# Kernel optimization log

Measured on AMD Instinct MI355X. Metric: run time of the kernel, lower is better.

## Reference

```python
import jax, jax.numpy as jnp
from jax import lax
import numpy as np

KSIZE = 3      # match-patch size
STRIDE = 1
RATE = 2       # down/up-sampling rate
FUSE_K = 3
SCALE = 10.0   # softmax scale
DN = ('NHWC', 'HWIO', 'NHWC')


def extract_patches(x, k, s):
    """tf.image.extract_patches(..., padding='SAME'); returns [B, L, k, k, C]."""
    B, H, W, C = x.shape
    oh, ow = -(-H // s), -(-W // s)
    ph = max((oh - 1) * s + k - H, 0)
    pw = max((ow - 1) * s + k - W, 0)
    xp = jnp.pad(x, ((0, 0), (ph // 2, ph - ph // 2), (pw // 2, pw - pw // 2), (0, 0)))
    cols = [xp[:, i:i + oh * s:s, j:j + ow * s:s, :] for i in range(k) for j in range(k)]
    p = jnp.stack(cols, axis=3)                 # [B, oh, ow, k*k, C]
    return p.reshape(B, oh * ow, k, k, C)


def setup_inputs() -> dict:
    key = jax.random.key(0)
    k1, k2, k3 = jax.random.split(key, 3)
    B, H, W, C = 4, 96, 96, 64
    f = jax.random.normal(k1, (B, H, W, C), jnp.float32)
    b = jax.random.normal(k2, (B, H, W, C), jnp.float32)
    mask = jnp.zeros((B, H, W, 1), jnp.float32)          # 0 = no hole -> all patches valid
    fuse_weight = jax.random.normal(k3, (FUSE_K, FUSE_K, 1, 1), jnp.float32) * 0.3
    return {"f": f, "b": b, "mask": mask, "fuse_weight": fuse_weight}


def reference(f, b, mask, fuse_weight):
    B, H, W, C = f.shape
    kernel = 2 * RATE
    # deconv kernels from full-res background: [B, 4, 4, C, L]
    raw_w = extract_patches(b, kernel, RATE * STRIDE).transpose(0, 2, 3, 4, 1)
    fd = f[:, 1::2, 1::2, :]
    bd = b[:, 1::2, 1::2, :]
    md = mask[:, 1::2, 1::2, :]
    h, w_ = fd.shape[1], fd.shape[2]
    L = h * w_
    # matching kernels from downscaled background: [B, 3, 3, C, L]
    wk = extract_patches(bd, KSIZE, STRIDE).transpose(0, 2, 3, 4, 1)
    # mask patches -> per-patch validity mm: [B, L]
    mp = extract_patches(md, KSIZE, STRIDE)
    mm = (jnp.mean(mp, axis=(2, 3, 4)) == 0.0).astype(f.dtype)

    def per_sample(xi, wi, rwi, mmi):
        # xi: [h, w, C]; wi: [3,3,C,L]; rwi: [4,4,C,L]; mmi: [L]
        norm = jnp.maximum(jnp.sqrt(jnp.sum(wi * wi, axis=(0, 1, 2))), 1e-4)
        yi = lax.conv_general_dilated(xi[None], wi / norm, (1, 1), 'SAME',
                                      dimension_numbers=DN)[0]        # [h, w, L]
        # fuse: 3x3 conv over flattened [HW, HW] score map, twice (transposed view)
        y = yi.reshape(1, L, L, 1)
        y = lax.conv_general_dilated(y, fuse_weight, (1, 1), 'SAME', dimension_numbers=DN)
        y = y.reshape(h, w_, h, w_).transpose(1, 0, 3, 2).reshape(1, L, L, 1)
        y = lax.conv_general_dilated(y, fuse_weight, (1, 1), 'SAME', dimension_numbers=DN)
        y = y.reshape(w_, h, w_, h).transpose(1, 0, 3, 2).reshape(h, w_, L)
        # mask-gated scaled softmax over background patches
        y = y * mmi
        y = jax.nn.softmax(y * SCALE, axis=-1) * mmi
        # deconv-style combine with raw 4x4 patches, stride=rate
        out = lax.conv_transpose(y[None], rwi, (RATE, RATE), 'SAME',
                                 dimension_numbers=DN, transpose_kernel=True)[0] / 4.0
        return out                                                    # [H, W, C]

    return jax.vmap(per_sample)(fd, wk, raw_w, mm)
```

## Files before the change

kernel.cpp:

```cpp
#include <hip/hip_runtime.h>
#include <hip/hip_bf16.h>

#define KL  2304
#define KC  64
#define KHS 48
#define KHH 96
#define OFFY (KHS*(KL + 1))

typedef __attribute__((ext_vector_type(8))) short bf16x8;
typedef __attribute__((ext_vector_type(4))) short bf16x4;
typedef __attribute__((ext_vector_type(8))) _Float16 f16x8;
typedef __attribute__((ext_vector_type(4))) _Float16 f16x4;
typedef __attribute__((ext_vector_type(4))) float f32x4;

static __device__ inline unsigned short f2bf(float x) {
    __hip_bfloat16 h = __float2bfloat16(x);
    return *reinterpret_cast<unsigned short*>(&h);
}
static __device__ inline float bf2f(unsigned short u) {
    unsigned v = ((unsigned)u) << 16;
    return __uint_as_float(v);
}
static __device__ inline unsigned short f2h(float x) {
    _Float16 h = (_Float16)x;
    return *reinterpret_cast<unsigned short*>(&h);
}
static __device__ inline float h2f(unsigned short u) {
    _Float16 h = *reinterpret_cast<_Float16*>(&u);
    return (float)h;
}

__global__ __launch_bounds__(64) void k_prep2(const float* __restrict__ f,
    const float* __restrict__ bsrc, const float* __restrict__ mask,
    float* __restrict__ nbuf, float* __restrict__ mdd,
    unsigned short* __restrict__ Ahat, unsigned short* __restrict__ Bhat)
{
    int blk = blockIdx.x;
    int p = blk % KL, bi = blk / KL;
    int y = p / KHS, x = p % KHS;
    int fy = 2*y + 1;
    int c = threadIdx.x;
    unsigned short* Ap = Ahat + ((size_t)bi*KL + p)*192;
    unsigned short* Bp = Bhat + ((size_t)bi*KL + p)*192;
    float bc = 0.f;
    #pragma unroll
    for (int dxi = 0; dxi < 3; dxi++) {
        int xx = x + dxi - 1;
        float av = 0.f, bv = 0.f;
        if ((unsigned)xx < KHS) {
            int fxx = 2*xx + 1;
            size_t src = (((size_t)bi*KHH + fy)*KHH + fxx)*KC + c;
            av = f[src]; bv = bsrc[src];
        }
        if (dxi == 1) bc = bv;
        Ap[dxi*64 + c] = f2h(av);
        Bp[dxi*64 + c] = f2h(bv);
    }
    float s = bc*bc;
    #pragma unroll
    for (int off = 32; off > 0; off >>= 1) s += __shfl_down(s, off);
    if (c == 0) {
        nbuf[bi*KL + p] = s;
        mdd[bi*KL + p]  = mask[((size_t)bi*KHH + fy)*KHH + (2*x + 1)];
    }
}

__global__ __launch_bounds__(256) void k_normmask(const float* __restrict__ nbuf,
    const float* __restrict__ mdd, float* __restrict__ rnrm, float* __restrict__ mm)
{
    int i = blockIdx.x*256 + threadIdx.x;
    int q = i % KL, bi = i / KL;
    int v = q / KHS, u = q % KHS;
    float sn = 0.f, sm = 0.f;
    for (int dy = -1; dy <= 1; dy++) {
        int vv = v + dy; if ((unsigned)vv >= KHS) continue;
        for (int dx = -1; dx <= 1; dx++) {
            int uu = u + dx; if ((unsigned)uu >= KHS) continue;
            sn += nbuf[bi*KL + vv*KHS + uu];
            sm += mdd[bi*KL + vv*KHS + uu];
        }
    }
    rnrm[i] = 1.0f / fmaxf(sqrtf(sn), 1e-4f);
    mm[i]   = (sm == 0.0f) ? 1.0f : 0.0f;
}

template<int KITERS, int OUTMODE, bool INFP16>
__global__ __launch_bounds__(256) void k_mfma_bt(const unsigned short* __restrict__ A,
    const unsigned short* __restrict__ B, void* __restrict__ Cv,
    int Ncols, size_t sA, size_t sB, size_t sC, int KDIM, int nsplit, size_t psize)
{
    int flat = blockIdx.x + gridDim.x*(blockIdx.y + gridDim.y*blockIdx.z);
    int nxy = gridDim.x*gridDim.y;
    int per = (nxy*gridDim.z) >> 3;
    int g = (flat & 7)*per + (flat >> 3);
    int z = g / nxy; int r = g - z*nxy;
    int by = r / gridDim.x; int bx = r - by*gridDim.x;

    int ks = z % nsplit, bi = z / nsplit;
    int kbase = ks * KITERS * 32;
    int n0 = bx*128, m0 = by*128;
    const unsigned short* Ab = A + (size_t)bi*sA;
    const unsigned short* Bb = B + (size_t)bi*sB;
    __shared__ unsigned short As[128*32];
    __shared__ unsigned short Bs[128*32];
    int t = threadIdx.x;
    int lane = t & 63, w = t >> 6;
    int l15 = lane & 15, quad = lane >> 4;
    int swf = (l15 >> 2) & 3;
    int wm = (w >> 1)*64, wn = (w & 1)*64;
    int srow = lane >> 2;
    int ch = lane & 3;
    f32x4 acc[4][4];
    #pragma unroll
    for (int i = 0; i < 4; i++)
        #pragma unroll
        for (int j = 0; j < 4; j++) acc[i][j] = (f32x4){0.f,0.f,0.f,0.f};

    for (int kk = 0; kk < KITERS; kk++) {
        int k0 = kbase + kk*32;
        #pragma unroll
        for (int i = 0; i < 2; i++) {
            int rbase = w*32 + i*16;
            int r2 = rbase + srow;
            int cs = (ch ^ ((r2 >> 2) & 3))*8;
            const unsigned short* ga = &Ab[(size_t)(m0 + r2)*KDIM + k0 + cs];
            __builtin_amdgcn_global_load_lds(
                (const __attribute__((address_space(1))) void*)ga,
                (__attribute__((address_space(3))) void*)&As[rbase*32], 16, 0, 0);
            const unsigned short* gb = &Bb[(size_t)(n0 + r2)*KDIM + k0 + cs];
            __builtin_amdgcn_global_load_lds(
                (const __attribute__((address_space(1))) void*)gb,
                (__attribute__((address_space(3))) void*)&Bs[rbase*32], 16, 0, 0);
        }
        __syncthreads();
        if (INFP16) {
            f16x8 af[4], bfr[4];
            #pragma unroll
            for (int mi = 0; mi < 4; mi++)
                af[mi] = *(const f16x8*)&As[(wm + mi*16 + l15)*32 + ((quad ^ swf)*8)];
            #pragma unroll
            for (int ni = 0; ni < 4; ni++)
                bfr[ni] = *(const f16x8*)&Bs[(wn + ni*16 + l15)*32 + ((quad ^ swf)*8)];
            #pragma unroll
            for (int mi = 0; mi < 4; mi++)
                #pragma unroll
                for (int ni = 0; ni < 4; ni++)
                    acc[mi][ni] = __builtin_amdgcn_mfma_f32_16x16x32_f16(
                        af[mi], bfr[ni], acc[mi][ni], 0, 0, 0);
        } else {
            bf16x8 af[4], bfr[4];
            #pragma unroll
            for (int mi = 0; mi < 4; mi++)
                af[mi] = *(const bf16x8*)&As[(wm + mi*16 + l15)*32 + ((quad ^ swf)*8)];
            #pragma unroll
            for (int ni = 0; ni < 4; ni++)
                bfr[ni] = *(const bf16x8*)&Bs[(wn + ni*16 + l15)*32 + ((quad ^ swf)*8)];
            #pragma unroll
            for (int mi = 0; mi < 4; mi++)
                #pragma unroll
                for (int ni = 0; ni < 4; ni++)
                    acc[mi][ni] = __builtin_amdgcn_mfma_f32_16x16x32_bf16(
                        af[mi], bfr[ni], acc[mi][ni], 0, 0, 0);
        }
        __syncthreads();
    }
    if (OUTMODE == 1 || OUTMODE == 2) {
        unsigned short* Cb = (unsigned short*)Cv + (size_t)ks*psize + (size_t)bi*sC;
        #pragma unroll
        for (int mi = 0; mi < 4; mi++)
            #pragma unroll
            for (int ni = 0; ni < 4; ni++) {
                int col = n0 + wn + ni*16 + l15;
                #pragma unroll
                for (int r2 = 0; r2 < 4; r2++) {
                    int row = m0 + wm + mi*16 + quad*4 + r2;
                    Cb[(size_t)row*Ncols + col] = (OUTMODE == 1)
                        ? f2bf(acc[mi][ni][r2]) : f2h(acc[mi][ni][r2]);
                }
            }
    } else {
        float* Cb = (float*)Cv + (size_t)ks*psize + (size_t)bi*sC;
        #pragma unroll
        for (int mi = 0; mi < 4; mi++)
            #pragma unroll
            for (int ni = 0; ni < 4; ni++) {
                int col = n0 + wn + ni*16 + l15;
                #pragma unroll
                for (int r2 = 0; r2 < 4; r2++) {
                    int row = m0 + wm + mi*16 + quad*4 + r2;
                    Cb[(size_t)row*Ncols + col] = acc[mi][ni][r2];
                }
            }
    }
}

#define STG(gb, lt, ktile, h) do {                                             \
    const unsigned short* _g = (gb) + (size_t)(h)*128*2304 + (size_t)(ktile)*64;\
    __builtin_amdgcn_global_load_lds(                                          \
        (const __attribute__((address_space(1))) void*)(_g),                   \
        (__attribute__((address_space(3))) void*)&(lt)[(ktile)&1][((h)*128 + (w<<3))*64], 16, 0, 0); \
    __builtin_amdgcn_global_load_lds(                                          \
        (const __attribute__((address_space(1))) void*)(_g + (size_t)64*2304), \
        (__attribute__((address_space(3))) void*)&(lt)[(ktile)&1][((h)*128 + 64 + (w<<3))*64], 16, 0, 0); \
} while (0)

#define MFMA_B(a, b, c) __builtin_amdgcn_mfma_f32_16x16x32_bf16(a, b, c, 0, 0, 0)

#define PHASE_SYNC_PRE()                                      \
    __builtin_amdgcn_s_barrier();                             \
    asm volatile("s_waitcnt lgkmcnt(0)" ::: "memory");        \
    __builtin_amdgcn_sched_barrier(0);                        \
    __builtin_amdgcn_s_setprio(1);

#define PHASE_SYNC_POST()                                     \
    __builtin_amdgcn_s_setprio(0);                            \
    __builtin_amdgcn_s_barrier();

__global__ __launch_bounds__(512, 2) void k_p8(
    const unsigned short* __restrict__ A,
    const unsigned short* __restrict__ B,
    unsigned short* __restrict__ C,
    size_t psize)
{
    __shared__ unsigned short Atile[2][16384];
    __shared__ unsigned short Btile[2][16384];

    int flat = blockIdx.x + gridDim.x*(blockIdx.y + gridDim.y*blockIdx.z);
    int nwg = gridDim.x*gridDim.y*gridDim.z;
    int qq = nwg >> 3, rr8 = nwg & 7;
    int xcd = flat & 7, sub = flat >> 3;
    int g = (xcd < rr8 ? xcd*(qq+1) : rr8*(qq+1) + (xcd - rr8)*qq) + sub;
    int nxy = gridDim.x*gridDim.y;
    int z = g / nxy; int rg = g - z*nxy;
    int by = rg / gridDim.x; int bx = rg - by*gridDim.x;

    int ks = z % 3, bi = z / 3;
    int kbase = ks * 768;
    int m0 = by * 256, n0 = bx * 256;
    const unsigned short* Ab = A + (size_t)bi * (2304ull*2304);
    const unsigned short* Bb = B + (size_t)bi * (1024ull*2304);

    int t = threadIdx.x;
    int w = t >> 6, lane = t & 63;
    int wr = w >> 2, wc = w & 3;
    int l15 = lane & 15, quad = lane >> 4, l7 = lane & 7;

    int rsub = t >> 3;
    int scol = ((t & 7) ^ (rsub & 7)) << 3;
    const unsigned short* gA = Ab + (size_t)(m0 + rsub)*2304 + kbase + scol;
    const unsigned short* gB = Bb + (size_t)(n0 + rsub)*2304 + kbase + scol;

    int sw0 = ((quad) ^ l7) << 3;
    int sw1 = ((4 + quad) ^ l7) << 3;
    int aBase = (wr*128 + l15)*64;
    int bBase = (wc*64  + l15)*64;

    f32x4 acc[8][4];
    #pragma unroll
    for (int mi = 0; mi < 8; mi++)
        #pragma unroll
        for (int ni = 0; ni < 4; ni++) acc[mi][ni] = (f32x4){0.f,0.f,0.f,0.f};

    STG(gA, Atile, 0, 0); STG(gA, Atile, 0, 1);
    STG(gB, Btile, 0, 0); STG(gB, Btile, 0, 1);
    STG(gA, Atile, 1, 0);
    asm volatile("s_waitcnt vmcnt(2)" ::: "memory");
    __builtin_amdgcn_s_barrier();

    bf16x8 af[4][2], bv[4][2];

    for (int kt = 0; kt < 12; kt++) {
        const unsigned short* At = &Atile[kt & 1][0];
        const unsigned short* Bt = &Btile[kt & 1][0];

        #pragma unroll
        for (int mi = 0; mi < 4; mi++) {
            af[mi][0] = *(const bf16x8*)&At[aBase + mi*1024 + sw0];
            af[mi][1] = *(const bf16x8*)&At[aBase + mi*1024 + sw1];
        }
        #pragma unroll
        for (int ni = 0; ni < 2; ni++) {
            bv[ni][0] = *(const bf16x8*)&Bt[bBase + ni*1024 + sw0];
            bv[ni][1] = *(const bf16x8*)&Bt[bBase + ni*1024 + sw1];
        }
        if (kt < 11) STG(gA, Atile, kt+1, 1);
        PHASE_SYNC_PRE();
        #pragma unroll
        for (int mi = 0; mi < 4; mi++)
            #pragma unroll
            for (int ni = 0; ni < 2; ni++) {
                acc[mi][ni] = MFMA_B(af[mi][0], bv[ni][0], acc[mi][ni]);
                acc[mi][ni] = MFMA_B(af[mi][1], bv[ni][1], acc[mi][ni]);
            }
        PHASE_SYNC_POST();

        #pragma unroll
        for (int ni = 2; ni < 4; ni++) {
            bv[ni][0] = *(const bf16x8*)&Bt[bBase + ni*1024 + sw0];
            bv[ni][1] = *(const bf16x8*)&Bt[bBase + ni*1024 + sw1];
        }
        if (kt < 11) STG(gB, Btile, kt+1, 0);
        PHASE_SYNC_PRE();
        #pragma unroll
        for (int mi = 0; mi < 4; mi++)
            #pragma unroll
            for (int ni = 2; ni < 4; ni++) {
                acc[mi][ni] = MFMA_B(af[mi][0], bv[ni][0], acc[mi][ni]);
                acc[mi][ni] = MFMA_B(af[mi][1], bv[ni][1], acc[mi][ni]);
            }
        PHASE_SYNC_POST();

        #pragma unroll
        for (int mi = 0; mi < 4; mi++) {
            af[mi][0] = *(const bf16x8*)&At[aBase + (4+mi)*1024 + sw0];
            af[mi][1] = *(const bf16x8*)&At[aBase + (4+mi)*1024 + sw1];
        }
        if (kt < 11) STG(gB, Btile, kt+1, 1);
        PHASE_SYNC_PRE();
        #pragma unroll
        for (int mi = 0; mi < 4; mi++)
            #pragma unroll
            for (int ni = 0; ni < 2; ni++) {
                acc[4+mi][ni] = MFMA_B(af[mi][0], bv[ni][0], acc[4+mi][ni]);
                acc[4+mi][ni] = MFMA_B(af[mi][1], bv[ni][1], acc[4+mi][ni]);
            }
        PHASE_SYNC_POST();

        if (kt < 10) {
            STG(gA, Atile, kt+2, 0);
            asm volatile("s_waitcnt vmcnt(2)" ::: "memory");
        } else {
            asm volatile("s_waitcnt vmcnt(0)" ::: "memory");
        }
        __builtin_amdgcn_s_barrier();
        __builtin_amdgcn_s_setprio(1);
        #pragma unroll
        for (int mi = 0; mi < 4; mi++)
            #pragma unroll
            for (int ni = 2; ni < 4; ni++) {
                acc[4+mi][ni] = MFMA_B(af[mi][0], bv[ni][0], acc[4+mi][ni]);
                acc[4+mi][ni] = MFMA_B(af[mi][1], bv[ni][1], acc[4+mi][ni]);
            }
        PHASE_SYNC_POST();
    }

    unsigned short* Cb = C + (size_t)ks*psize + (size_t)bi*(2304ull*1024);
    #pragma unroll
    for (int mi = 0; mi < 8; mi++)
        #pragma unroll
        for (int ni = 0; ni < 4; ni++) {
            int col = n0 + wc*64 + ni*16 + l15;
            int rowb = m0 + wr*128 + mi*16 + quad*4;
            #pragma unroll
            for (int r = 0; r < 4; r++)
                Cb[(size_t)(rowb + r)*1024 + col] = f2bf(acc[mi][ni][r]);
        }
}

__global__ __launch_bounds__(256) void k_fuse_a2(const unsigned short* __restrict__ T,
    const float* __restrict__ rnrm, const float* __restrict__ fw,
    unsigned short* __restrict__ Y1)
{
    __shared__ float Sl[10][280];
    int bi = blockIdx.z;
    int qt = blockIdx.x;
    int p0 = blockIdx.y*8, q0 = qt*256;
    const unsigned short* Tb = T + (size_t)bi*KL*KL;
    const float* rn = rnrm + bi*KL;
    int t = threadIdx.x;
    bool edge = (qt == 0) | (qt == 8);
    if (!edge) {
        for (int idx = t; idx < 10*34; idx += 256) {
            int r = idx / 34, j = idx - r*34;
            int pp = p0 - 1 + r;
            int qq0 = q0 - 8 + j*8;
            float s[8];
            #pragma unroll
            for (int k = 0; k < 8; k++) s[k] = 0.f;
            if ((unsigned)pp < KL) {
                size_t base = (size_t)pp*KL + qq0;
                bool bm = (pp >= KHS), bp = (pp < KL - KHS);
                size_t offm = bm ? (size_t)OFFY : 0;
                size_t offp = bp ? (size_t)OFFY : 0;
                float fm = bm ? 1.f : 0.f, fp2 = bp ? 1.f : 0.f;
                f16x8 v0 = *(const f16x8*)&Tb[base];
                f16x8 vm = *(const f16x8*)&Tb[base - offm];
                f16x8 vp = *(const f16x8*)&Tb[base + offp];
                #pragma unroll
                for (int k = 0; k < 8; k++)
                    s[k] = ((float)v0[k] + fm*(float)vm[k] + fp2*(float)vp[k]) * rn[qq0 + k];
            }
            #pragma unroll
            for (int k = 0; k < 8; k++) Sl[r][j*8 + k] = s[k];
        }
    } else {
        for (int idx = t; idx < 10*272; idx += 256) {
            int r = idx / 272, c = idx - r*272;
            int pp = p0 - 1 + r, qq = q0 - 8 + c;
            float s = 0.f;
            if ((unsigned)pp < KL && (unsigned)qq < KL) {
                size_t base = (size_t)pp*KL + qq;
                float acc = h2f(Tb[base]);
                if (pp >= KHS && qq >= KHS)         acc += h2f(Tb[base - OFFY]);
                if (pp < KL - KHS && qq < KL - KHS) acc += h2f(Tb[base + OFFY]);
                s = acc * rn[qq];
            }
            Sl[r][c] = s;
        }
    }
    __syncthreads();
    float w[9];
    #pragma unroll
    for (int i = 0; i < 9; i++) w[i] = fw[i];
    int q = q0 + t;
    float h0[10], h1[10], h2[10];
    #pragma unroll
    for (int r = 0; r < 10; r++) {
        float s0 = Sl[r][t+7], s1 = Sl[r][t+8], s2 = Sl[r][t+9];
        h0[r] = w[0]*s0 + w[1]*s1 + w[2]*s2;
        h1[r] = w[3]*s0 + w[4]*s1 + w[5]*s2;
        h2[r] = w[6]*s0 + w[7]*s1 + w[8]*s2;
    }
    #pragma unroll
    for (int rr = 0; rr < 8; rr++) {
        Y1[((size_t)bi*KL + p0 + rr)*KL + q] = f2h(h0[rr] + h1[rr+1] + h2[rr+2]);
    }
}

__global__ __launch_bounds__(256) void k_fuse_b(const unsigned short* __restrict__ Y1,
    const float* __restrict__ fw, const float* __restrict__ mm,
    unsigned short* __restrict__ Ybf)
{
    __shared__ float rowb[4][KL];
    __shared__ float red[8];
    int blk = blockIdx.x;
    int tp0 = (blk % 1152)*2;
    int bi  = blk / 1152;
    int t = threadIdx.x;
    const unsigned short* Yb = Y1 + (size_t)bi*KL*KL;
    #pragma unroll
    for (int a = 0; a < 4; a++) {
        int t2 = tp0 - 1 + a;
        if ((unsigned)t2 < KL) {
            int pr = (t2 % KHS)*KHS + t2/KHS;
            const f16x8* src = (const f16x8*)&Yb[(size_t)pr*KL];
            for (int i = t; i < KL/8; i += 256) {
                f16x8 v = src[i];
                #pragma unroll
                for (int j = 0; j < 8; j++) rowb[a][i*8 + j] = (float)v[j];
            }
        } else {
            float4 z = {0.f,0.f,0.f,0.f};
            float4* dst = (float4*)&rowb[a][0];
            for (int i = t; i < KL/4; i += 256) dst[i] = z;
        }
    }
    float w9[9];
    #pragma unroll
    for (int i = 0; i < 9; i++) w9[i] = fw[i];
    __syncthreads();
    int w = t >> 6, lane = t & 63;
    int half = w >> 1;
    int l128 = t & 127;
    int tp = tp0 + half;
    int x = tp / KHS, y = tp - x*KHS;
    int p = y*KHS + x;
    const float* mmb = mm + bi*KL;
    float vals[18];
    float lmax = -1e30f;
    #pragma unroll
    for (int i = 0; i < 18; i++) {
        int q = l128 + i*128;
        int qm = (q >= KHS)      ? q - KHS : 2255 + q;
        int qp = (q <= KL-1-KHS) ? q + KHS : q - 2255;
        float fm = (q != 0)    ? 1.f : 0.f;
        float fp = (q != KL-1) ? 1.f : 0.f;
        float am = w9[0]*rowb[half][qm] + w9[3]*rowb[half+1][qm] + w9[6]*rowb[half+2][qm];
        float a0 = w9[1]*rowb[half][q]  + w9[4]*rowb[half+1][q]  + w9[7]*rowb[half+2][q];
        float ap = w9[2]*rowb[half][qp] + w9[5]*rowb[half+1][qp] + w9[8]*rowb[half+2][qp];
        float val = (fm*am + a0 + fp*ap) * mmb[q] * 10.0f;
        vals[i] = val;
        lmax = fmaxf(lmax, val);
    }
    #pragma unroll
    for (int off = 32; off > 0; off >>= 1) lmax = fmaxf(lmax, __shfl_down(lmax, off));
    if (lane == 0) red[w] = lmax;
    __syncthreads();
    lmax = fmaxf(red[half*2], red[half*2 + 1]);
    float lsum = 0.f;
    #pragma unroll
    for (int i = 0; i < 18; i++) {
        float e = __expf(vals[i] - lmax);
        vals[i] = e;
        lsum += e;
    }
    #pragma unroll
    for (int off = 32; off > 0; off >>= 1) lsum += __shfl_down(lsum, off);
    if (lane == 0) red[4 + w] = lsum;
    __syncthreads();
    lsum = red[4 + half*2] + red[4 + half*2 + 1];
    float inv = 1.0f / lsum;
    unsigned short* orow = Ybf + ((size_t)bi*KL + p)*KL;
    #pragma unroll
    for (int i = 0; i < 18; i++) {
        int q = l128 + i*128;
        orow[q] = f2bf(vals[i]*inv*mmb[q]);
    }
}

__global__ __launch_bounds__(256) void k_buildRt(const float* __restrict__ bsrc,
    unsigned short* __restrict__ Rt)
{
    int idx = blockIdx.x*256 + threadIdx.x;
    int k8 = idx % 288;
    int rest = idx / 288;
    int n  = rest % 1024;
    int bi = rest / 1024;
    int jj = n >> 6, c = n & 63;
    int ky = jj >> 2, kx = jj & 3;
    int k0 = k8*8;
    bf16x8 vv;
    #pragma unroll
    for (int j = 0; j < 8; j++) {
        int q = k0 + j;
        int v = q / KHS, u = q % KHS;
        int ry = 2*v + ky - 1, rx = 2*u + kx - 1;
        float val = 0.f;
        if ((unsigned)ry < KHH && (unsigned)rx < KHH)
            val = bsrc[(((size_t)bi*KHH + ry)*KHH + rx)*KC + c];
        vv[j] = (short)f2bf(val);
    }
    *(bf16x8*)&Rt[((size_t)bi*1024 + n)*KL + k0] = vv;
}

__global__ __launch_bounds__(256) void k_overlap(const unsigned short* __restrict__ P,
    float* __restrict__ out, size_t psize)
{
    size_t gid = (size_t)blockIdx.x*256 + threadIdx.x;
    int c4 = (int)(gid & 15)*4;
    size_t r = gid >> 4;
    int ix = (int)(r % KHH); r /= KHH;
    int iy = (int)(r % KHH);
    int bi = (int)(r / KHH);
    f32x4 acc = (f32x4){0.f,0.f,0.f,0.f};
    #pragma unroll
    for (int sy = 0; sy < 2; sy++) {
        int ky = (iy & 1) ? (sy*2) : (sy*2 + 1);
        int yp = (iy + 1 - ky) >> 1;
        if ((unsigned)yp >= KHS) continue;
        #pragma unroll
        for (int sx = 0; sx < 2; sx++) {
            int kx = (ix & 1) ? (sx*2) : (sx*2 + 1);
            int xp = (ix + 1 - kx) >> 1;
            if ((unsigned)xp >= KHS) continue;
            size_t idx = (((size_t)bi*KL + yp*KHS + xp)*16 + (ky*4 + kx))*64 + c4;
            #pragma unroll
            for (int s = 0; s < 3; s++) {
                bf16x4 v = *(const bf16x4*)&P[idx + s*psize];
                #pragma unroll
                for (int j = 0; j < 4; j++)
                    acc[j] += bf2f((unsigned short)v[j]);
            }
        }
    }
    f32x4 o = acc * 0.25f;
    *(f32x4*)&out[(((size_t)bi*KHH + iy)*KHH + ix)*KC + c4] = o;
}

extern "C" void kernel_launch(void* const* d_in, const int* in_sizes, int n_in,
                              void* d_out, int out_size, void* d_ws, size_t ws_size,
                              hipStream_t stream)
{
    const float* f    = (const float*)d_in[0];
    const float* b    = (const float*)d_in[1];
    const float* mask = (const float*)d_in[2];
    const float* fw   = (const float*)d_in[3];
    float* out = (float*)d_out;

    auto need = [](int nbc) -> size_t {
        return (size_t)nbc * (2ull*KL*KC + 4ull*KL + 2ull*(size_t)KL*KL) * 4ull;
    };
    int nbc = 4;
    if (need(nbc) > ws_size) nbc = 2;
    if (need(nbc) > ws_size) nbc = 1;

    for (int bi0 = 0; bi0 < 4; bi0 += nbc) {
        int nb = (4 - bi0 < nbc) ? (4 - bi0) : nbc;
        const float* fc = f    + (size_t)bi0*KHH*KHH*KC;
        const float* bc = b    + (size_t)bi0*KHH*KHH*KC;
        const float* mc = mask + (size_t)bi0*KHH*KHH;
        float* outc = out + (size_t)bi0*KHH*KHH*KC;

        float* w    = (float*)d_ws;
        float* nbuf = w;  w += (size_t)nbc*KL;
        float* mdd  = w;  w += (size_t)nbc*KL;
        float* rnrm = w;  w += (size_t)nbc*KL;
        float* mmb  = w;  w += (size_t)nbc*KL;
        float* bufA = w;  w += (size_t)nbc*KL*KL;
        float* bufB = w;
        unsigned short* Ahat = (unsigned short*)bufB;
        unsigned short* Bhat = Ahat + (size_t)nbc*KL*192;
        unsigned short* Tbuf = (unsigned short*)bufA;
        unsigned short* Y1   = (unsigned short*)bufB;
        unsigned short* Ybf = (unsigned short*)bufA;
        unsigned short* Rtb = Ybf + (size_t)nbc*KL*KL;
        unsigned short* Pbuf = (unsigned short*)bufB;
        size_t psize = (size_t)nbc*KL*1024;

        k_prep2     <<<nb*KL, 64, 0, stream>>>(fc, bc, mc, nbuf, mdd, Ahat, Bhat);
        k_normmask  <<<(nb*KL)/256, 256, 0, stream>>>(nbuf, mdd, rnrm, mmb);
        k_mfma_bt<6,2,true><<<dim3(18, 18, nb), 256, 0, stream>>>(
            Ahat, Bhat, Tbuf, KL, (size_t)KL*192, (size_t)KL*192, (size_t)KL*KL,
            192, 1, 0);
        k_fuse_a2   <<<dim3(9, 288, nb), 256, 0, stream>>>(Tbuf, rnrm, fw, Y1);
        k_fuse_b    <<<nb*1152, 256, 0, stream>>>(Y1, fw, mmb, Ybf);
        k_buildRt   <<<(nb*1024*288)/256, 256, 0, stream>>>(bc, Rtb);
        k_p8<<<dim3(4, 9, nb*3), 512, 0, stream>>>(Ybf, Rtb, Pbuf, psize);
        k_overlap   <<<nb*KL/4*16/16, 256, 0, stream>>>(Pbuf, outc, psize);
    }
}
```

Before: 284.0 us.

## Restructure GEMM main loop into 4-stage K=32 pipeline with register double-buffering

Rewrites the k_p8 bf16 GEMM main loop to use 32-wide K tiles in a 4-deep LDS ring, prefetching three tiles ahead. B fragments are ping-ponged between two register sets so the next tile's LDS reads overlap the current MFMAs. This replaces the previous 2-stage, 64-wide K tiles and their four barrier-delimited phases. The XOR swizzle is dropped in favour of a plain 32-element row layout, which may bring back LDS bank conflicts. The 2-way MFMA unrolling per phase also becomes a single-K MFMA per fragment.

```diff
diff --git a/kernel.cpp b/kernel.cpp
--- a/kernel.cpp
+++ b/kernel.cpp
@@ -194,27 +194,59 @@
     }
 }
 
-#define STG(gb, lt, ktile, h) do {                                             \
-    const unsigned short* _g = (gb) + (size_t)(h)*128*2304 + (size_t)(ktile)*64;\
+#define STGA4(tt, j) do {                                                      \
     __builtin_amdgcn_global_load_lds(                                          \
-        (const __attribute__((address_space(1))) void*)(_g),                   \
-        (__attribute__((address_space(3))) void*)&(lt)[(ktile)&1][((h)*128 + (w<<3))*64], 16, 0, 0); \
+        (const __attribute__((address_space(1))) void*)(gA + (size_t)(j)*128*2304 + (size_t)(tt)*32), \
+        (__attribute__((address_space(3))) void*)&Atile[(tt)&3][((j)*128 + (w<<4))*32], 16, 0, 0); \
+} while (0)
+#define STGB4(tt, j) do {                                                      \
     __builtin_amdgcn_global_load_lds(                                          \
-        (const __attribute__((address_space(1))) void*)(_g + (size_t)64*2304), \
-        (__attribute__((address_space(3))) void*)&(lt)[(ktile)&1][((h)*128 + 64 + (w<<3))*64], 16, 0, 0); \
+        (const __attribute__((address_space(1))) void*)(gB + (size_t)(j)*128*2304 + (size_t)(tt)*32), \
+        (__attribute__((address_space(3))) void*)&Btile[(tt)&3][((j)*128 + (w<<4))*32], 16, 0, 0); \
 } while (0)
 
 #define MFMA_B(a, b, c) __builtin_amdgcn_mfma_f32_16x16x32_bf16(a, b, c, 0, 0, 0)
 
-#define PHASE_SYNC_PRE()                                      \
-    __builtin_amdgcn_s_barrier();                             \
-    asm volatile("s_waitcnt lgkmcnt(0)" ::: "memory");        \
-    __builtin_amdgcn_sched_barrier(0);                        \
-    __builtin_amdgcn_s_setprio(1);
-
-#define PHASE_SYNC_POST()                                     \
-    __builtin_amdgcn_s_setprio(0);                            \
-    __builtin_amdgcn_s_barrier();
+#define KT_BODY(kt, BVU, BVF) do {                                             \
+    const unsigned short* At = &Atile[(kt) & 3][0];                            \
+                                                          \
+    __builtin_amdgcn_s_barrier();                                              \
+    _Pragma("unroll")                                                          \
+    for (int i = 0; i < 4; i++)                                                \
+        af1[i] = *(const bf16x8*)&At[aOff + 2048 + i*512];                     \
+    if ((kt) + 3 < 24) { STGA4((kt)+3, 0); STGA4((kt)+3, 1); }                 \
+    __builtin_amdgcn_s_setprio(1);                                             \
+    _Pragma("unroll")                                                          \
+    for (int mi = 0; mi < 4; mi++)                                             \
+        _Pragma("unroll")                                                      \
+        for (int ni = 0; ni < 4; ni++)                                         \
+            acc[mi][ni] = MFMA_B(af0[mi], BVU[ni], acc[mi][ni]);               \
+    __builtin_amdgcn_s_setprio(0);                                             \
+                                                          \
+    __builtin_amdgcn_s_barrier();                                              \
+    if ((kt) < 23) {                                                           \
+        if ((kt) <= 20)      asm volatile("s_waitcnt vmcnt(6)" ::: "memory");  \
+        else if ((kt) == 21) asm volatile("s_waitcnt vmcnt(4)" ::: "memory");  \
+        else                 asm volatile("s_waitcnt vmcnt(0)" ::: "memory");  \
+        __builtin_amdgcn_sched_barrier(0);                                     \
+        const unsigned short* An = &Atile[((kt)+1) & 3][0];                    \
+        const unsigned short* Bn = &Btile[((kt)+1) & 3][0];                    \
+        _Pragma("unroll")                                                      \
+        for (int i = 0; i < 4; i++)                                            \
+            af0[i] = *(const bf16x8*)&An[aOff + i*512];                        \
+        _Pragma("unroll")                                                      \
+        for (int ni = 0; ni < 4; ni++)                                         \
+            BVF[ni] = *(const bf16x8*)&Bn[bOff + ni*512];                      \
+    }                                                                          \
+    if ((kt) + 3 < 24) { STGB4((kt)+3, 0); STGB4((kt)+3, 1); }                 \
+    __builtin_amdgcn_s_setprio(1);                                             \
+    _Pragma("unroll")                                                          \
+    for (int mi = 0; mi < 4; mi++)                                             \
+        _Pragma("unroll")                                                      \
+        for (int ni = 0; ni < 4; ni++)                                         \
+            acc[4+mi][ni] = MFMA_B(af1[mi], BVU[ni], acc[4+mi][ni]);           \
+    __builtin_amdgcn_s_setprio(0);                                             \
+} while (0)
 
 __global__ __launch_bounds__(512, 2) void k_p8(
     const unsigned short* __restrict__ A,
@@ -222,8 +254,8 @@
     unsigned short* __restrict__ C,
     size_t psize)
 {
-    __shared__ unsigned short Atile[2][16384];
-    __shared__ unsigned short Btile[2][16384];
+    __shared__ unsigned short Atile[4][8192];
+    __shared__ unsigned short Btile[4][8192];
 
     int flat = blockIdx.x + gridDim.x*(blockIdx.y + gridDim.y*blockIdx.z);
     int nwg = gridDim.x*gridDim.y*gridDim.z;
@@ -243,17 +275,13 @@
     int t = threadIdx.x;
     int w = t >> 6, lane = t & 63;
     int wr = w >> 2, wc = w & 3;
-    int l15 = lane & 15, quad = lane >> 4, l7 = lane & 7;
-
-    int rsub = t >> 3;
-    int scol = ((t & 7) ^ (rsub & 7)) << 3;
-    const unsigned short* gA = Ab + (size_t)(m0 + rsub)*2304 + kbase + scol;
-    const unsigned short* gB = Bb + (size_t)(n0 + rsub)*2304 + kbase + scol;
-
-    int sw0 = ((quad) ^ l7) << 3;
-    int sw1 = ((4 + quad) ^ l7) << 3;
-    int aBase = (wr*128 + l15)*64;
-    int bBase = (wc*64  + l15)*64;
+    int l15 = lane & 15, quad = lane >> 4;
+
+    const unsigned short* gA = Ab + (size_t)(m0 + (t >> 2))*2304 + kbase + (t & 3)*8;
+    const unsigned short* gB = Bb + (size_t)(n0 + (t >> 2))*2304 + kbase + (t & 3)*8;
+
+    int aOff = (wr*128 + l15)*32 + quad*8;
+    int bOff = (wc*64  + l15)*32 + quad*8;
 
     f32x4 acc[8][4];
     #pragma unroll
@@ -261,87 +289,27 @@
         #pragma unroll
         for (int ni = 0; ni < 4; ni++) acc[mi][ni] = (f32x4){0.f,0.f,0.f,0.f};
 
-    STG(gA, Atile, 0, 0); STG(gA, Atile, 0, 1);
-    STG(gB, Btile, 0, 0); STG(gB, Btile, 0, 1);
-    STG(gA, Atile, 1, 0);
-    asm volatile("s_waitcnt vmcnt(2)" ::: "memory");
+    #pragma unroll
+    for (int tt = 0; tt < 3; tt++) {
+        STGA4(tt, 0); STGA4(tt, 1);
+        STGB4(tt, 0); STGB4(tt, 1);
+    }
+    asm volatile("s_waitcnt vmcnt(8)" ::: "memory");
     __builtin_amdgcn_s_barrier();
 
-    bf16x8 af[4][2], bv[4][2];
-
-    for (int kt = 0; kt < 12; kt++) {
-        const unsigned short* At = &Atile[kt & 1][0];
-        const unsigned short* Bt = &Btile[kt & 1][0];
-
-        #pragma unroll
-        for (int mi = 0; mi < 4; mi++) {
-            af[mi][0] = *(const bf16x8*)&At[aBase + mi*1024 + sw0];
-            af[mi][1] = *(const bf16x8*)&At[aBase + mi*1024 + sw1];
-        }
-        #pragma unroll
-        for (int ni = 0; ni < 2; ni++) {
-            bv[ni][0] = *(const bf16x8*)&Bt[bBase + ni*1024 + sw0];
-            bv[ni][1] = *(const bf16x8*)&Bt[bBase + ni*1024 + sw1];
-        }
-        if (kt < 11) STG(gA, Atile, kt+1, 1);
-        PHASE_SYNC_PRE();
-        #pragma unroll
-        for (int mi = 0; mi < 4; mi++)
-            #pragma unroll
-            for (int ni = 0; ni < 2; ni++) {
-                acc[mi][ni] = MFMA_B(af[mi][0], bv[ni][0], acc[mi][ni]);
-                acc[mi][ni] = MFMA_B(af[mi][1], bv[ni][1], acc[mi][ni]);
-            }
-        PHASE_SYNC_POST();
-
-        #pragma unroll
-        for (int ni = 2; ni < 4; ni++) {
-            bv[ni][0] = *(const bf16x8*)&Bt[bBase + ni*1024 + sw0];
-            bv[ni][1] = *(const bf16x8*)&Bt[bBase + ni*1024 + sw1];
-        }
-        if (kt < 11) STG(gB, Btile, kt+1, 0);
-        PHASE_SYNC_PRE();
-        #pragma unroll
-        for (int mi = 0; mi < 4; mi++)
-            #pragma unroll
-            for (int ni = 2; ni < 4; ni++) {
-                acc[mi][ni] = MFMA_B(af[mi][0], bv[ni][0], acc[mi][ni]);
-                acc[mi][ni] = MFMA_B(af[mi][1], bv[ni][1], acc[mi][ni]);
-            }
-        PHASE_SYNC_POST();
-
-        #pragma unroll
-        for (int mi = 0; mi < 4; mi++) {
-            af[mi][0] = *(const bf16x8*)&At[aBase + (4+mi)*1024 + sw0];
-            af[mi][1] = *(const bf16x8*)&At[aBase + (4+mi)*1024 + sw1];
-        }
-        if (kt < 11) STG(gB, Btile, kt+1, 1);
-        PHASE_SYNC_PRE();
-        #pragma unroll
-        for (int mi = 0; mi < 4; mi++)
-            #pragma unroll
-            for (int ni = 0; ni < 2; ni++) {
-                acc[4+mi][ni] = MFMA_B(af[mi][0], bv[ni][0], acc[4+mi][ni]);
-                acc[4+mi][ni] = MFMA_B(af[mi][1], bv[ni][1], acc[4+mi][ni]);
-            }
-        PHASE_SYNC_POST();
-
-        if (kt < 10) {
-            STG(gA, Atile, kt+2, 0);
-            asm volatile("s_waitcnt vmcnt(2)" ::: "memory");
-        } else {
-            asm volatile("s_waitcnt vmcnt(0)" ::: "memory");
-        }
-        __builtin_amdgcn_s_barrier();
-        __builtin_amdgcn_s_setprio(1);
-        #pragma unroll
-        for (int mi = 0; mi < 4; mi++)
-            #pragma unroll
-            for (int ni = 2; ni < 4; ni++) {
-                acc[4+mi][ni] = MFMA_B(af[mi][0], bv[ni][0], acc[4+mi][ni]);
-                acc[4+mi][ni] = MFMA_B(af[mi][1], bv[ni][1], acc[4+mi][ni]);
-            }
-        PHASE_SYNC_POST();
+    bf16x8 af0[4], af1[4], bvA[4], bvB[4];
+    #pragma unroll
+    for (int i = 0; i < 4; i++)
+        af0[i] = *(const bf16x8*)&Atile[0][aOff + i*512];
+    #pragma unroll
+    for (int ni = 0; ni < 4; ni++)
+        bvA[ni] = *(const bf16x8*)&Btile[0][bOff + ni*512];
+
+    #pragma unroll 1
+    for (int ktp = 0; ktp < 12; ktp++) {
+        int kt0 = ktp*2;
+        KT_BODY(kt0,     bvA, bvB);
+        KT_BODY(kt0 + 1, bvB, bvA);
     }
 
     unsigned short* Cb = C + (size_t)ks*psize + (size_t)bi*(2304ull*1024);
```

Result: no change. 284.0 us (+0.0%).
